# Performance work log

Hardware: AMD Instinct MI355X
Metric: run time of the kernel (lower is better)

The kernel has to match this reference:

```python
import jax, jax.numpy as jnp
import numpy as np


def conv1x1(x, w, b):
    # x: [B,Cin,H,W], w: [Cout,Cin], b: [Cout]
    return jnp.einsum('bchw,oc->bohw', x, w) + b[None, :, None, None]


def setup_inputs() -> dict:
    key = jax.random.key(0)
    ks = jax.random.split(key, 10)
    B, Cm, C, H, W = 4, 6, 64, 64, 64
    map1 = jax.random.normal(ks[0], (B, Cm, H, W), jnp.float32)
    map2 = jax.random.normal(ks[1], (B, Cm, H, W), jnp.float32)
    feature_map = jax.random.normal(ks[2], (B, C, H, W), jnp.float32)
    # 1x1 conv params (kaiming-ish scale)
    wb = jax.random.normal(ks[3], (Cm, Cm), jnp.float32) / np.sqrt(Cm)
    bb = jnp.zeros((Cm,), jnp.float32)
    wc = jax.random.normal(ks[4], (Cm, Cm), jnp.float32) / np.sqrt(Cm)
    bc = jnp.zeros((Cm,), jnp.float32)
    wd = jax.random.normal(ks[5], (C, C), jnp.float32) / np.sqrt(C)
    bd = jnp.zeros((C,), jnp.float32)
    alpha = jnp.zeros((1,), jnp.float32)
    return {"map1": map1, "map2": map2, "feature_map": feature_map,
            "wb": wb, "bb": bb, "wc": wc, "bc": bc, "wd": wd, "bd": bd,
            "alpha": alpha}


def reference(map1, map2, feature_map, wb, bb, wc, bc, wd, bd, alpha):
    B, _, H, W = map1.shape
    N = H * W
    # conv1x1 projections, flatten spatial
    feat_b = conv1x1(map1, wb, bb).reshape(B, -1, N).transpose(0, 2, 1)  # [B,N,6]
    feat_c = conv1x1(map2, wc, bc).reshape(B, -1, N)                      # [B,6,N]
    attention_s = jax.nn.softmax(jnp.einsum('bnc,bcm->bnm', feat_b, feat_c), axis=-1)  # [B,N,N]
    feat_d = conv1x1(feature_map, wd, bd).reshape(B, -1, N)               # [B,C,N]
    # bmm with attention_s^T: out[b,c,n] = sum_m feat_d[b,c,m] * attn[b,n,m]
    feat_e = jnp.einsum('bcm,bnm->bcn', feat_d, attention_s).reshape(B, -1, H, W)
    return alpha * feat_e + feature_map
```

## Files before the change

kernel.cpp:

```cpp
#include <hip/hip_runtime.h>
#include <hip/hip_bf16.h>
#include <math.h>


#define BATCH 4
#define CMAP  6
#define CH    64
#define NSP   4096
#define TN    64
#define PSTR  72

typedef __attribute__((ext_vector_type(8))) short short8;
typedef __attribute__((ext_vector_type(4))) float f32x4;

#if __has_builtin(__builtin_amdgcn_exp2f)
#define EXP2(x) __builtin_amdgcn_exp2f(x)
#else
#define EXP2(x) exp2f(x)
#endif

__device__ __forceinline__ unsigned f2bf(float f) {
    unsigned u = __float_as_uint(f);
    return (u + 0x7fffu + ((u >> 16) & 1u)) >> 16;
}

#define INVLN2 1.44269504088896f
#define SHIFT_BF16 0xC238u
#define ONE_BF16   0x3F80u


__global__ void proj_kernel(const float* __restrict__ map1, const float* __restrict__ map2,
                            const float* __restrict__ fm,
                            const float* __restrict__ wb, const float* __restrict__ bb,
                            const float* __restrict__ wc, const float* __restrict__ bc,
                            const float* __restrict__ wd, const float* __restrict__ bd,
                            unsigned short* __restrict__ featq8,
                            unsigned short* __restrict__ featk8,
                            unsigned short* __restrict__ featdf)
{
    __shared__ unsigned short vfrag[2048];

    const int b    = blockIdx.z;
    const int half = blockIdx.y;
    const int lane = threadIdx.x & 63;
    const int og   = threadIdx.x >> 6;
    const int n    = blockIdx.x * 64 + lane;

    const int ht = lane >> 5;
    const int mm = lane & 31;
    const int q4 = mm >> 3, jj = mm & 7;
    const int cb_local = og >> 1;
    float vals[CH];
#pragma unroll
    for (int c = 0; c < CH; ++c)
        vals[c] = fm[(size_t)(b*CH + c)*NSP + n];
#pragma unroll
    for (int oi = 0; oi < 8; ++oi) {
        const int o = half*32 + og*8 + oi;
        float a = bd[o];
#pragma unroll
        for (int c = 0; c < CH; ++c)
            a = fmaf(vals[c], wd[o*CH + c], a);
        const int r = (og & 1)*8 + oi;
        vfrag[(ht*2 + cb_local)*512 + (q4*16 + r)*8 + jj] = (unsigned short)f2bf(a);
    }

    if (half == 0 && og == 0) {
        float v1[CMAP], v2[CMAP];
#pragma unroll
        for (int c = 0; c < CMAP; ++c) {
            v1[c] = map1[(size_t)(b*CMAP + c)*NSP + n];
            v2[c] = map2[(size_t)(b*CMAP + c)*NSP + n];
        }
        unsigned qv[CMAP], kv[CMAP];
#pragma unroll
        for (int o = 0; o < CMAP; ++o) {
            float a1 = bb[o], a2 = bc[o];
#pragma unroll
            for (int c = 0; c < CMAP; ++c) {
                a1 = fmaf(v1[c], wb[o*CMAP + c], a1);
                a2 = fmaf(v2[c], wc[o*CMAP + c], a2);
            }
            qv[o] = f2bf(a1 * INVLN2);
            kv[o] = f2bf(a2);
        }
        uint4 qw, kw;
        qw.x = qv[0] | (qv[1] << 16);
        qw.y = qv[2] | (qv[3] << 16);
        qw.z = qv[4] | (qv[5] << 16);
        qw.w = SHIFT_BF16;
        kw.x = kv[0] | (kv[1] << 16);
        kw.y = kv[2] | (kv[3] << 16);
        kw.z = kv[4] | (kv[5] << 16);
        kw.w = ONE_BF16;
        *(uint4*)&featq8[(size_t)(b*NSP + n)*8] = qw;
        *(uint4*)&featk8[(size_t)(b*NSP + n)*8] = kw;
    }

    __syncthreads();

    {
        const int tt = threadIdx.x;
        const uint4 d = *(const uint4*)&vfrag[tt*8];
        const int ht2 = tt >> 7, inner = tt & 127;
        const size_t off = (((size_t)(b*128 + blockIdx.x*2 + ht2)*4) + half*2)*512
                         + (size_t)inner*8;
        *(uint4*)&featdf[off] = d;
    }
}

__global__ __launch_bounds__(256, 2)
void attn_kernel(const unsigned short* __restrict__ featq8,
                 const unsigned short* __restrict__ featk8,
                 const unsigned short* __restrict__ featdf,
                 const float* __restrict__ fm, const float* __restrict__ alpha_p,
                 float* __restrict__ out)
{
    __shared__ unsigned short p_scr[2][4][16*PSTR];
    __shared__ float l_scr[4][16];

    const int b    = blockIdx.z;
    const int chh  = blockIdx.y;
    const int t    = threadIdx.x;
    const int lane = t & 63, w = t >> 6;
    const int row16 = lane & 15, quad = lane >> 4;
    const int n0w  = blockIdx.x * 64 + w * 16;

    short8 qf = {0,0,0,0,0,0,0,0};
    if (quad == 0)
        qf = *(const short8*)&featq8[(size_t)(b*NSP + n0w + row16)*8];

    const unsigned short* kbase = featk8 + ((size_t)b*NSP + row16)*8 + quad*8;
    const unsigned short* vfb = featdf + ((size_t)b*128*4)*512 + lane*8;
    const int cb0 = chh*2, cb1 = chh*2 + 1;

    short8 k0 = *(const short8*)(kbase +  0*8);
    short8 k1 = *(const short8*)(kbase + 16*8);
    short8 k2 = *(const short8*)(kbase + 32*8);
    short8 k3 = *(const short8*)(kbase + 48*8);
    short8 v00 = *(const short8*)(vfb + (size_t)(0*4 + cb0)*512);
    short8 v01 = *(const short8*)(vfb + (size_t)(1*4 + cb0)*512);
    short8 v10 = *(const short8*)(vfb + (size_t)(0*4 + cb1)*512);
    short8 v11 = *(const short8*)(vfb + (size_t)(1*4 + cb1)*512);

    const f32x4 zf = {0.f,0.f,0.f,0.f};
    f32x4 acc0 = zf, acc1 = zf;
    float lacc = 0.f;
    const int prow = row16 * PSTR;

#pragma unroll 2
    for (int tile = 0; tile < NSP/TN; ++tile) {
        f32x4 s0 = __builtin_amdgcn_mfma_f32_16x16x32_bf16(k0, qf, zf, 0, 0, 0);
        f32x4 s1 = __builtin_amdgcn_mfma_f32_16x16x32_bf16(k1, qf, zf, 0, 0, 0);
        f32x4 s2 = __builtin_amdgcn_mfma_f32_16x16x32_bf16(k2, qf, zf, 0, 0, 0);
        f32x4 s3 = __builtin_amdgcn_mfma_f32_16x16x32_bf16(k3, qf, zf, 0, 0, 0);

        const int tn = (tile + 1) & (NSP/TN - 1);
        const int m1 = tn * TN;
        const short8 k0n = *(const short8*)(kbase + (m1 +  0)*8);
        const short8 k1n = *(const short8*)(kbase + (m1 + 16)*8);
        const short8 k2n = *(const short8*)(kbase + (m1 + 32)*8);
        const short8 k3n = *(const short8*)(kbase + (m1 + 48)*8);
        const short8 v00n = *(const short8*)(vfb + (size_t)((tn*2 + 0)*4 + cb0)*512);
        const short8 v01n = *(const short8*)(vfb + (size_t)((tn*2 + 1)*4 + cb0)*512);
        const short8 v10n = *(const short8*)(vfb + (size_t)((tn*2 + 0)*4 + cb1)*512);
        const short8 v11n = *(const short8*)(vfb + (size_t)((tn*2 + 1)*4 + cb1)*512);

        unsigned short* pw = &p_scr[tile & 1][w][prow + quad*4];
#define PAM_DO(mb, sv)                                                          \
        {                                                                       \
            const float p0 = EXP2(sv[0]), p1 = EXP2(sv[1]);                     \
            const float p2 = EXP2(sv[2]), p3 = EXP2(sv[3]);                     \
            lacc += (p0 + p1) + (p2 + p3);                                      \
            uint2 pp;                                                           \
            pp.x = __builtin_amdgcn_perm(__float_as_uint(p1), __float_as_uint(p0), 0x07060302u); \
            pp.y = __builtin_amdgcn_perm(__float_as_uint(p3), __float_as_uint(p2), 0x07060302u); \
            *(uint2*)(pw + mb*16) = pp;                                         \
        }
        PAM_DO(0, s0) PAM_DO(1, s1) PAM_DO(2, s2) PAM_DO(3, s3)
#undef PAM_DO

        const unsigned short* pr = &p_scr[tile & 1][w][prow + quad*8];
        const short8 a0 = *(const short8*)pr;
        const short8 a1 = *(const short8*)(pr + 32);

        acc0 = __builtin_amdgcn_mfma_f32_16x16x32_bf16(a0, v00, acc0, 0, 0, 0);
        acc0 = __builtin_amdgcn_mfma_f32_16x16x32_bf16(a1, v01, acc0, 0, 0, 0);
        acc1 = __builtin_amdgcn_mfma_f32_16x16x32_bf16(a0, v10, acc1, 0, 0, 0);
        acc1 = __builtin_amdgcn_mfma_f32_16x16x32_bf16(a1, v11, acc1, 0, 0, 0);

        k0 = k0n; k1 = k1n; k2 = k2n; k3 = k3n;
        v00 = v00n; v01 = v01n; v10 = v10n; v11 = v11n;
    }

    lacc += __shfl_xor(lacc, 16);
    lacc += __shfl_xor(lacc, 32);
    if (quad == 0) l_scr[w][row16] = lacc;
    const float4 lv = *(const float4*)&l_scr[w][quad*4];

    const float alpha = alpha_p[0];
    const float c0 = alpha / (lv.x + 1e-30f);
    const float c1 = alpha / (lv.y + 1e-30f);
    const float c2 = alpha / (lv.z + 1e-30f);
    const float c3 = alpha / (lv.w + 1e-30f);
#pragma unroll
    for (int cb = 0; cb < 2; ++cb) {
        const int ch = chh*32 + cb*16 + row16;
        const size_t base = (size_t)(b*CH + ch)*NSP + n0w + quad*4;
        const float4 f = *(const float4*)&fm[base];
        const f32x4 a = cb ? acc1 : acc0;
        float4 o;
        o.x = fmaf(c0, a[0], f.x);
        o.y = fmaf(c1, a[1], f.y);
        o.z = fmaf(c2, a[2], f.z);
        o.w = fmaf(c3, a[3], f.w);
        *(float4*)&out[base] = o;
    }
}

extern "C" void kernel_launch(void* const* d_in, const int* in_sizes, int n_in,
                              void* d_out, int out_size, void* d_ws, size_t ws_size,
                              hipStream_t stream)
{
    const float* map1  = (const float*)d_in[0];
    const float* map2  = (const float*)d_in[1];
    const float* fm    = (const float*)d_in[2];
    const float* wb    = (const float*)d_in[3];
    const float* bb    = (const float*)d_in[4];
    const float* wc    = (const float*)d_in[5];
    const float* bc    = (const float*)d_in[6];
    const float* wd    = (const float*)d_in[7];
    const float* bd    = (const float*)d_in[8];
    const float* alpha = (const float*)d_in[9];
    float* out = (float*)d_out;

    unsigned short* featq8 = (unsigned short*)d_ws;
    unsigned short* featk8 = featq8 + (size_t)BATCH*NSP*8;
    unsigned short* featdf = featk8 + (size_t)BATCH*NSP*8;

    proj_kernel<<<dim3(NSP/64, 2, BATCH), 256, 0, stream>>>(
        map1, map2, fm, wb, bb, wc, bc, wd, bd, featq8, featk8, featdf);
    attn_kernel<<<dim3(NSP/64, 2, BATCH), 256, 0, stream>>>(
        featq8, featk8, featdf, fm, alpha, out);
}
```

Before: 125.5 us.

## Software-pipeline PV MFMA one tile behind QK exp to overlap LDS round trip

Restructures the attention loop into a prologue, a steady state and an epilogue. The PV matrix products for tile t-1 now run while tile t's scores are exponentiated and written to shared memory, so the write-then-read of P through LDS no longer sits directly on the MFMA dependency chain. V fragments are double-buffered one tile further ahead. This costs more live registers (an extra set of V and score values), which could reduce occupancy or cause spills.

Result: faster. 122.6 us (-2.3%).

```diff
diff --git a/kernel.cpp b/kernel.cpp
--- a/kernel.cpp
+++ b/kernel.cpp
@@ -134,64 +134,98 @@
     const unsigned short* vfb = featdf + ((size_t)b*128*4)*512 + lane*8;
     const int cb0 = chh*2, cb1 = chh*2 + 1;
 
+    const f32x4 zf = {0.f,0.f,0.f,0.f};
+    f32x4 acc0 = zf, acc1 = zf;
+    float lacc = 0.f;
+    const int prow = row16 * PSTR;
+
+#define PAM_DO(pwp, mb, sv)                                                     \
+    {                                                                           \
+        const float p0 = EXP2(sv[0]), p1 = EXP2(sv[1]);                         \
+        const float p2 = EXP2(sv[2]), p3 = EXP2(sv[3]);                         \
+        lacc += (p0 + p1) + (p2 + p3);                                          \
+        uint2 pp;                                                               \
+        pp.x = __builtin_amdgcn_perm(__float_as_uint(p1), __float_as_uint(p0), 0x07060302u); \
+        pp.y = __builtin_amdgcn_perm(__float_as_uint(p3), __float_as_uint(p2), 0x07060302u); \
+        *(uint2*)((pwp) + (mb)*16) = pp;                                        \
+    }
+
     short8 k0 = *(const short8*)(kbase +  0*8);
     short8 k1 = *(const short8*)(kbase + 16*8);
     short8 k2 = *(const short8*)(kbase + 32*8);
     short8 k3 = *(const short8*)(kbase + 48*8);
-    short8 v00 = *(const short8*)(vfb + (size_t)(0*4 + cb0)*512);
-    short8 v01 = *(const short8*)(vfb + (size_t)(1*4 + cb0)*512);
-    short8 v10 = *(const short8*)(vfb + (size_t)(0*4 + cb1)*512);
-    short8 v11 = *(const short8*)(vfb + (size_t)(1*4 + cb1)*512);
-
-    const f32x4 zf = {0.f,0.f,0.f,0.f};
-    f32x4 acc0 = zf, acc1 = zf;
-    float lacc = 0.f;
-    const int prow = row16 * PSTR;
+    short8 vn0 = *(const short8*)(vfb + (size_t)(0*4 + cb0)*512);
+    short8 vn1 = *(const short8*)(vfb + (size_t)(1*4 + cb0)*512);
+    short8 vn2 = *(const short8*)(vfb + (size_t)(0*4 + cb1)*512);
+    short8 vn3 = *(const short8*)(vfb + (size_t)(1*4 + cb1)*512);
+
+    f32x4 s0 = __builtin_amdgcn_mfma_f32_16x16x32_bf16(k0, qf, zf, 0, 0, 0);
+    f32x4 s1 = __builtin_amdgcn_mfma_f32_16x16x32_bf16(k1, qf, zf, 0, 0, 0);
+    f32x4 s2 = __builtin_amdgcn_mfma_f32_16x16x32_bf16(k2, qf, zf, 0, 0, 0);
+    f32x4 s3 = __builtin_amdgcn_mfma_f32_16x16x32_bf16(k3, qf, zf, 0, 0, 0);
+    {
+        unsigned short* pw = &p_scr[0][w][prow + quad*4];
+        PAM_DO(pw, 0, s0) PAM_DO(pw, 1, s1) PAM_DO(pw, 2, s2) PAM_DO(pw, 3, s3)
+    }
+    k0 = *(const short8*)(kbase + (64 +  0)*8);
+    k1 = *(const short8*)(kbase + (64 + 16)*8);
+    k2 = *(const short8*)(kbase + (64 + 32)*8);
+    k3 = *(const short8*)(kbase + (64 + 48)*8);
+    short8 vv0 = vn0, vv1 = vn1, vv2 = vn2, vv3 = vn3;
+    vn0 = *(const short8*)(vfb + (size_t)((2 + 0)*4 + cb0)*512);
+    vn1 = *(const short8*)(vfb + (size_t)((2 + 1)*4 + cb0)*512);
+    vn2 = *(const short8*)(vfb + (size_t)((2 + 0)*4 + cb1)*512);
+    vn3 = *(const short8*)(vfb + (size_t)((2 + 1)*4 + cb1)*512);
 
 #pragma unroll 2
-    for (int tile = 0; tile < NSP/TN; ++tile) {
-        f32x4 s0 = __builtin_amdgcn_mfma_f32_16x16x32_bf16(k0, qf, zf, 0, 0, 0);
-        f32x4 s1 = __builtin_amdgcn_mfma_f32_16x16x32_bf16(k1, qf, zf, 0, 0, 0);
-        f32x4 s2 = __builtin_amdgcn_mfma_f32_16x16x32_bf16(k2, qf, zf, 0, 0, 0);
-        f32x4 s3 = __builtin_amdgcn_mfma_f32_16x16x32_bf16(k3, qf, zf, 0, 0, 0);
-
-        const int tn = (tile + 1) & (NSP/TN - 1);
-        const int m1 = tn * TN;
-        const short8 k0n = *(const short8*)(kbase + (m1 +  0)*8);
-        const short8 k1n = *(const short8*)(kbase + (m1 + 16)*8);
-        const short8 k2n = *(const short8*)(kbase + (m1 + 32)*8);
-        const short8 k3n = *(const short8*)(kbase + (m1 + 48)*8);
-        const short8 v00n = *(const short8*)(vfb + (size_t)((tn*2 + 0)*4 + cb0)*512);
-        const short8 v01n = *(const short8*)(vfb + (size_t)((tn*2 + 1)*4 + cb0)*512);
-        const short8 v10n = *(const short8*)(vfb + (size_t)((tn*2 + 0)*4 + cb1)*512);
-        const short8 v11n = *(const short8*)(vfb + (size_t)((tn*2 + 1)*4 + cb1)*512);
-
-        unsigned short* pw = &p_scr[tile & 1][w][prow + quad*4];
-#define PAM_DO(mb, sv)                                                          \
-        {                                                                       \
-            const float p0 = EXP2(sv[0]), p1 = EXP2(sv[1]);                     \
-            const float p2 = EXP2(sv[2]), p3 = EXP2(sv[3]);                     \
-            lacc += (p0 + p1) + (p2 + p3);                                      \
-            uint2 pp;                                                           \
-            pp.x = __builtin_amdgcn_perm(__float_as_uint(p1), __float_as_uint(p0), 0x07060302u); \
-            pp.y = __builtin_amdgcn_perm(__float_as_uint(p3), __float_as_uint(p2), 0x07060302u); \
-            *(uint2*)(pw + mb*16) = pp;                                         \
-        }
-        PAM_DO(0, s0) PAM_DO(1, s1) PAM_DO(2, s2) PAM_DO(3, s3)
-#undef PAM_DO
-
-        const unsigned short* pr = &p_scr[tile & 1][w][prow + quad*8];
+    for (int tc = 1; tc < NSP/TN; ++tc) {
+        const int par = tc & 1;
+
+        s0 = __builtin_amdgcn_mfma_f32_16x16x32_bf16(k0, qf, zf, 0, 0, 0);
+        s1 = __builtin_amdgcn_mfma_f32_16x16x32_bf16(k1, qf, zf, 0, 0, 0);
+        s2 = __builtin_amdgcn_mfma_f32_16x16x32_bf16(k2, qf, zf, 0, 0, 0);
+        s3 = __builtin_amdgcn_mfma_f32_16x16x32_bf16(k3, qf, zf, 0, 0, 0);
+
+        const int kn = ((tc + 1) & (NSP/TN - 1)) * TN;
+        const short8 k0n = *(const short8*)(kbase + (kn +  0)*8);
+        const short8 k1n = *(const short8*)(kbase + (kn + 16)*8);
+        const short8 k2n = *(const short8*)(kbase + (kn + 32)*8);
+        const short8 k3n = *(const short8*)(kbase + (kn + 48)*8);
+
+        const unsigned short* pr = &p_scr[par ^ 1][w][prow + quad*8];
         const short8 a0 = *(const short8*)pr;
         const short8 a1 = *(const short8*)(pr + 32);
 
-        acc0 = __builtin_amdgcn_mfma_f32_16x16x32_bf16(a0, v00, acc0, 0, 0, 0);
-        acc0 = __builtin_amdgcn_mfma_f32_16x16x32_bf16(a1, v01, acc0, 0, 0, 0);
-        acc1 = __builtin_amdgcn_mfma_f32_16x16x32_bf16(a0, v10, acc1, 0, 0, 0);
-        acc1 = __builtin_amdgcn_mfma_f32_16x16x32_bf16(a1, v11, acc1, 0, 0, 0);
+        {
+            unsigned short* pw = &p_scr[par][w][prow + quad*4];
+            PAM_DO(pw, 0, s0) PAM_DO(pw, 1, s1) PAM_DO(pw, 2, s2) PAM_DO(pw, 3, s3)
+        }
+
+        acc0 = __builtin_amdgcn_mfma_f32_16x16x32_bf16(a0, vv0, acc0, 0, 0, 0);
+        acc0 = __builtin_amdgcn_mfma_f32_16x16x32_bf16(a1, vv1, acc0, 0, 0, 0);
+        acc1 = __builtin_amdgcn_mfma_f32_16x16x32_bf16(a0, vv2, acc1, 0, 0, 0);
+        acc1 = __builtin_amdgcn_mfma_f32_16x16x32_bf16(a1, vv3, acc1, 0, 0, 0);
+
+        vv0 = vn0; vv1 = vn1; vv2 = vn2; vv3 = vn3;
+        const int vt = (tc + 1) & (NSP/TN - 1);
+        vn0 = *(const short8*)(vfb + (size_t)((vt*2 + 0)*4 + cb0)*512);
+        vn1 = *(const short8*)(vfb + (size_t)((vt*2 + 1)*4 + cb0)*512);
+        vn2 = *(const short8*)(vfb + (size_t)((vt*2 + 0)*4 + cb1)*512);
+        vn3 = *(const short8*)(vfb + (size_t)((vt*2 + 1)*4 + cb1)*512);
 
         k0 = k0n; k1 = k1n; k2 = k2n; k3 = k3n;
-        v00 = v00n; v01 = v01n; v10 = v10n; v11 = v11n;
-    }
+    }
+
+    {
+        const unsigned short* pr = &p_scr[1][w][prow + quad*8];
+        const short8 a0 = *(const short8*)pr;
+        const short8 a1 = *(const short8*)(pr + 32);
+        acc0 = __builtin_amdgcn_mfma_f32_16x16x32_bf16(a0, vv0, acc0, 0, 0, 0);
+        acc0 = __builtin_amdgcn_mfma_f32_16x16x32_bf16(a1, vv1, acc0, 0, 0, 0);
+        acc1 = __builtin_amdgcn_mfma_f32_16x16x32_bf16(a0, vv2, acc1, 0, 0, 0);
+        acc1 = __builtin_amdgcn_mfma_f32_16x16x32_bf16(a1, vv3, acc1, 0, 0, 0);
+    }
+#undef PAM_DO
 
     lacc += __shfl_xor(lacc, 16);
     lacc += __shfl_xor(lacc, 32);
```
